# Kernel tuning notes

Hardware: AMD Instinct MI355X
Metric: run time of the kernel (lower is better)

Reference implementation:

```python
import jax, jax.numpy as jnp
import numpy as np

EPS = 1e-6  # EPSILON in the original (undefined there; small stabilizer)
MS = 1      # max_shift_size
FEAT = 128  # memory_feature_size


def setup_inputs() -> dict:
    key = jax.random.key(0)
    ks = jax.random.split(key, 17)
    B, V, E, H, N, F = 64, 10000, 256, 512, 8192, FEAT
    G = 4 * H
    s = 0.02  # param init scale
    return {
        'x': jax.random.randint(ks[0], (B,), 0, V),
        'h': jax.random.normal(ks[1], (B, H)) * 0.1,
        'c': jax.random.normal(ks[2], (B, H)) * 0.1,
        'w_read': jax.random.uniform(ks[3], (B, N)),
        'w_write': jax.random.uniform(ks[4], (B, N)),
        'bank': jax.random.normal(ks[5], (B, N, F)),
        'emb': jax.random.normal(ks[6], (V, E)) * s,
        'W_ih': jax.random.normal(ks[7], (G, E)) * s,
        'b_ih': jnp.zeros((G,)),
        'W_hh': jax.random.normal(ks[8], (G, H)) * s,
        'b_hh': jnp.zeros((G,)),
        'W_read': jax.random.normal(ks[9], (134, H)) * s,
        'b_read': jnp.zeros((134,)),
        'W_write': jax.random.normal(ks[10], (390, H)) * s,
        'b_write': jnp.zeros((390,)),
        'W_out': jax.random.normal(ks[11], (V, F)) * s,
        'b_out': jnp.zeros((V,)),
    }


def _lstm_cell(xe, h, c, W_ih, b_ih, W_hh, b_hh):
    g = xe @ W_ih.T + b_ih + h @ W_hh.T + b_hh  # [B, 4H]
    i, f, gg, o = jnp.split(g, 4, axis=1)
    c2 = jax.nn.sigmoid(f) * c + jax.nn.sigmoid(i) * jnp.tanh(gg)
    h2 = jax.nn.sigmoid(o) * jnp.tanh(c2)
    return h2, c2


def _head_move(bank, w_prev, k, b, g, s, r):
    # content addressing: cosine similarity of key vs each memory row
    mE = bank + EPS                       # [B, N, F]
    kE = k[:, None, :] + EPS              # [B, 1, F]
    num = jnp.sum(mE * kE, axis=-1)       # [B, N]
    den = jnp.linalg.norm(mE, axis=-1) * jnp.linalg.norm(kE, axis=-1)
    sim = num / jnp.maximum(den, 1e-8)
    w = jax.nn.softmax(b * sim, axis=1)
    # interpolation (as written in the source: w + (1-g)*w_prev)
    w = w + (1.0 - g) * w_prev
    # circular shift by location addressing (vectorized conv over modulo pad)
    N = w.shape[1]
    idx = (jnp.arange(N)[:, None] + jnp.arange(-MS, MS + 1)[None, :]) % N  # [N, K]
    w = jnp.einsum('bnk,bk->bn', w[:, idx], s)
    # sharpen
    wr = w ** r
    return wr / (jnp.sum(wr, axis=1, keepdims=True) + EPS)


def _interpret_read(h, W, b):
    o = h @ W.T + b
    F = FEAT
    k = o[:, :F]
    beta = jax.nn.softplus(o[:, F:F + 1])
    g = jax.nn.sigmoid(o[:, F + 1:F + 2])
    s = jax.nn.softmax(o[:, F + 2:F + 2 + (2 * MS + 1)], axis=1)
    r = 1.0 + jax.nn.softplus(o[:, F + 2 + (2 * MS + 1):F + 3 + (2 * MS + 1)])
    return k, beta, g, s, r


def _interpret_write(h, W, b):
    o = h @ W.T + b
    F = FEAT
    k, beta, g, s, r = _interpret_read(h, W[:F + 3 + (2 * MS + 1)], b[:F + 3 + (2 * MS + 1)])
    base = F + 3 + (2 * MS + 1)
    e = jax.nn.sigmoid(o[:, base:base + F])
    a = o[:, base + F:base + 2 * F]
    return k, beta, g, s, r, e, a


def reference(x, h, c, w_read, w_write, bank, emb, W_ih, b_ih, W_hh, b_hh,
              W_read, b_read, W_write, b_write, W_out, b_out):
    # controller
    xe = emb[x]                                  # [B, E]
    h2, c2 = _lstm_cell(xe, h, c, W_ih, b_ih, W_hh, b_hh)
    # write head + memory write
    k, beta, g, s, r, e, a = _interpret_write(h2, W_write, b_write)
    ww = _head_move(bank, w_write, k, beta, g, s, r)   # [B, N]
    bank2 = bank * (1.0 - ww[:, :, None] * e[:, None, :]) + ww[:, :, None] * a[:, None, :]
    # read head + memory read (uses updated bank)
    k, beta, g, s, r = _interpret_read(h2, W_read, b_read)
    wr = _head_move(bank2, w_read, k, beta, g, s, r)
    rvec = jnp.sum(wr[:, :, None] * bank2, axis=1)     # [B, F]
    return rvec @ W_out.T + b_out                      # [B, V]
```

## Files before the change

kernel.cpp:

```cpp
#include <hip/hip_runtime.h>
#include <math.h>

#define BB   64
#define NN   8192
#define FF   128
#define HH   512
#define GG   2048
#define EE   256
#define VV   10000
#define EPSF 1e-6f

static constexpr size_t OFF_XT    = 0;
static constexpr size_t OFF_GPART = 49152;
static constexpr size_t OFF_H2T   = 311296;
static constexpr size_t OFF_HPART = 344064;
static constexpr size_t OFF_PAR   = 411136;
static constexpr size_t OFF_ZW    = 445952;
static constexpr size_t OFF_Q4    = 970240;
static constexpr size_t OFF_Q1    = 3067392;
static constexpr size_t OFF_WR    = 3591680;
static constexpr size_t OFF_WRWW  = 4115968;
static constexpr size_t OFF_PT    = 4640256;
static constexpr size_t OFF_T3    = 5164544;
static constexpr size_t OFF_RVEC  = 5164608;

__device__ __forceinline__ float sigmoidf_(float x){ return 1.f/(1.f + __expf(-x)); }
__device__ __forceinline__ float softplusf_(float x){ return (x > 20.f) ? x : log1pf(__expf(x)); }

__global__ __launch_bounds__(256) void gather_xt_kernel(
    const int* __restrict__ x, const float* __restrict__ h,
    const float* __restrict__ emb, float* __restrict__ Xt)
{
  const int idx = blockIdx.x*256 + threadIdx.x;
  const int k = idx >> 6, b = idx & 63;
  float v = (k < EE) ? emb[(size_t)x[b]*EE + k] : h[(size_t)b*HH + (k - EE)];
  Xt[(size_t)k*64 + b] = v;
}

__global__ __launch_bounds__(256) void lstm_gates_kernel(
    const float* __restrict__ Xt, const float* __restrict__ Wih,
    const float* __restrict__ Whh, float* __restrict__ gpart)
{
  const int tid = threadIdx.x;
  const int lane = tid & 63;
  const int gw = __builtin_amdgcn_readfirstlane(blockIdx.x*4 + (tid >> 6));
  const int jg = gw >> 1, kc = gw & 1;
  const int j0 = jg << 2;
  float a0=0.f, a1=0.f, a2=0.f, a3=0.f;
  if (kc == 0){
    const float* w0 = Wih + (size_t)(j0+0)*EE;
    const float* w1 = Wih + (size_t)(j0+1)*EE;
    const float* w2 = Wih + (size_t)(j0+2)*EE;
    const float* w3 = Wih + (size_t)(j0+3)*EE;
    #pragma unroll 4
    for (int k = 0; k < EE; ++k){
      const float xv = Xt[(size_t)k*64 + lane];
      a0 = fmaf(w0[k],xv,a0); a1 = fmaf(w1[k],xv,a1);
      a2 = fmaf(w2[k],xv,a2); a3 = fmaf(w3[k],xv,a3);
    }
    const float* v0 = Whh + (size_t)(j0+0)*HH;
    const float* v1 = Whh + (size_t)(j0+1)*HH;
    const float* v2 = Whh + (size_t)(j0+2)*HH;
    const float* v3 = Whh + (size_t)(j0+3)*HH;
    #pragma unroll 4
    for (int k = 0; k < 128; ++k){
      const float xv = Xt[(size_t)(EE+k)*64 + lane];
      a0 = fmaf(v0[k],xv,a0); a1 = fmaf(v1[k],xv,a1);
      a2 = fmaf(v2[k],xv,a2); a3 = fmaf(v3[k],xv,a3);
    }
  } else {
    const float* v0 = Whh + (size_t)(j0+0)*HH;
    const float* v1 = Whh + (size_t)(j0+1)*HH;
    const float* v2 = Whh + (size_t)(j0+2)*HH;
    const float* v3 = Whh + (size_t)(j0+3)*HH;
    #pragma unroll 4
    for (int k = 128; k < 512; ++k){
      const float xv = Xt[(size_t)(EE+k)*64 + lane];
      a0 = fmaf(v0[k],xv,a0); a1 = fmaf(v1[k],xv,a1);
      a2 = fmaf(v2[k],xv,a2); a3 = fmaf(v3[k],xv,a3);
    }
  }
  float* gp = gpart + (size_t)kc*131072 + (size_t)j0*64 + lane;
  gp[0] = a0; gp[64] = a1; gp[128] = a2; gp[192] = a3;
}

__global__ __launch_bounds__(256) void lstm_act_kernel(
    const float* __restrict__ gpart, const float* __restrict__ bih,
    const float* __restrict__ bhh, const float* __restrict__ c,
    float* __restrict__ h2t)
{
  const int idx = blockIdx.x*256 + threadIdx.x;
  const int bb = idx & 63, hh = idx >> 6;
  #define GSUM(j) (gpart[(size_t)(j)*64+bb] + gpart[(size_t)131072+(size_t)(j)*64+bb] + bih[j] + bhh[j])
  const float gi = GSUM(hh);
  const float gf = GSUM(512+hh);
  const float gg = GSUM(1024+hh);
  const float go = GSUM(1536+hh);
  #undef GSUM
  const float c0 = c[(size_t)bb*HH + hh];
  const float c2 = sigmoidf_(gf)*c0 + sigmoidf_(gi)*tanhf(gg);
  h2t[(size_t)hh*64 + bb] = sigmoidf_(go)*tanhf(c2);
}

__global__ __launch_bounds__(256) void head_gemm_kernel(
    const float* __restrict__ h2t, const float* __restrict__ Ww,
    const float* __restrict__ Wr, float* __restrict__ hpart)
{
  const int tid = threadIdx.x;
  const int lane = tid & 63;
  const int gw = __builtin_amdgcn_readfirstlane(blockIdx.x*4 + (tid >> 6));
  const int jg = gw >> 1, kc = gw & 1;
  if (jg >= 131) return;
  const int j0 = jg << 2;
  const float* w0 = (j0+0 < 390) ? (Ww + (size_t)(j0+0)*HH) : (Wr + (size_t)(j0+0-390)*HH);
  const float* w1 = (j0+1 < 390) ? (Ww + (size_t)(j0+1)*HH) : (Wr + (size_t)(j0+1-390)*HH);
  const float* w2 = (j0+2 < 390) ? (Ww + (size_t)(j0+2)*HH) : (Wr + (size_t)(j0+2-390)*HH);
  const float* w3 = (j0+3 < 390) ? (Ww + (size_t)(j0+3)*HH) : (Wr + (size_t)(j0+3-390)*HH);
  const int k0 = kc << 8;
  float a0=0.f, a1=0.f, a2=0.f, a3=0.f;
  #pragma unroll 4
  for (int k = k0; k < k0+256; ++k){
    const float xv = h2t[(size_t)k*64 + lane];
    a0 = fmaf(w0[k],xv,a0); a1 = fmaf(w1[k],xv,a1);
    a2 = fmaf(w2[k],xv,a2); a3 = fmaf(w3[k],xv,a3);
  }
  float* hp = hpart + (size_t)kc*33536 + (size_t)j0*64 + lane;
  hp[0] = a0; hp[64] = a1; hp[128] = a2; hp[192] = a3;
}

__global__ void interpret_kernel(const float* __restrict__ hp,
                                 const float* __restrict__ bw,
                                 const float* __restrict__ br,
                                 float* __restrict__ params)
{
  const int b = blockIdx.x, l = threadIdx.x;
  float* P = params + (size_t)b*544;
  #define OC(j) (hp[(size_t)(j)*64+b] + hp[(size_t)33536+(size_t)(j)*64+b])
  float skw = 0.f, skr = 0.f, sakr = 0.f, sa2 = 0.f;
  #pragma unroll
  for (int f = l; f < 128; f += 64){
    float kwE = OC(f) + bw[f] + EPSF;
    float ee  = sigmoidf_(OC(134+f) + bw[134+f]);
    float aa  = OC(262+f) + bw[262+f];
    float krE = OC(390+f) + br[f] + EPSF;
    P[f] = kwE; P[128+f] = krE; P[256+f] = aa; P[384+f] = ee;
    skw = fmaf(kwE,kwE,skw); skr = fmaf(krE,krE,skr);
    sakr = fmaf(aa,krE,sakr); sa2 = fmaf(aa,aa,sa2);
  }
  #pragma unroll
  for (int m = 32; m >= 1; m >>= 1){
    skw += __shfl_xor(skw,m); skr += __shfl_xor(skr,m);
    sakr += __shfl_xor(sakr,m); sa2 += __shfl_xor(sa2,m);
  }
  if (l == 0){
    P[512+0] = softplusf_(OC(128) + bw[128]);
    P[512+1] = sigmoidf_(OC(129) + bw[129]);
    {
      float x0 = OC(130)+bw[130], x1 = OC(131)+bw[131], x2 = OC(132)+bw[132];
      float mm = fmaxf(x0, fmaxf(x1, x2));
      float e0 = __expf(x0-mm), e1 = __expf(x1-mm), e2 = __expf(x2-mm);
      float s = e0+e1+e2;
      P[512+2] = e0/s; P[512+3] = e1/s; P[512+4] = e2/s;
    }
    P[512+5] = 1.f + softplusf_(OC(133) + bw[133]);
    P[512+6] = softplusf_(OC(518) + br[128]);
    P[512+7] = sigmoidf_(OC(519) + br[129]);
    {
      float x0 = OC(520)+br[130], x1 = OC(521)+br[131], x2 = OC(522)+br[132];
      float mm = fmaxf(x0, fmaxf(x1, x2));
      float e0 = __expf(x0-mm), e1 = __expf(x1-mm), e2 = __expf(x2-mm);
      float s = e0+e1+e2;
      P[512+8] = e0/s; P[512+9] = e1/s; P[512+10] = e2/s;
    }
    P[512+11] = 1.f + softplusf_(OC(523) + br[133]);
    P[512+12] = sqrtf(skw); P[512+13] = sqrtf(skr);
    P[512+14] = sakr;       P[512+15] = sa2;
  }
  #undef OC
}

__global__ __launch_bounds__(256) void pass_a_kernel(
    const float* __restrict__ bank, const float* __restrict__ params,
    float* __restrict__ zw, float4* __restrict__ q4, float* __restrict__ q1)
{
  const int blk = blockIdx.x;
  const int b = blk >> 5, chunk = blk & 31;
  const int tid = threadIdx.x;
  const int wv = tid >> 6, lane = tid & 63;
  const int fslot = lane & 7, rsub = lane >> 3;
  const float* P = params + (size_t)b*544;
  const int fb = fslot << 4;
  float kw[16], kr[16], av[16], ev[16];
  #pragma unroll
  for (int i = 0; i < 16; ++i){
    kw[i] = P[fb+i]; kr[i] = P[128+fb+i]; av[i] = P[256+fb+i]; ev[i] = P[384+fb+i];
  }
  const float beta_w = P[512+0], nkw = P[512+12];
  const float C_akr = P[512+14], Ca2 = P[512+15];
  for (int it = 0; it < 8; ++it){
    const int n = (chunk << 8) + (it << 5) + (wv << 3) + rsub;
    const size_t row = (size_t)b*NN + n;
    const float4* m4 = reinterpret_cast<const float4*>(bank + row*FF + fb);
    float mv[16];
    *reinterpret_cast<float4*>(&mv[0])  = m4[0];
    *reinterpret_cast<float4*>(&mv[4])  = m4[1];
    *reinterpret_cast<float4*>(&mv[8])  = m4[2];
    *reinterpret_cast<float4*>(&mv[12]) = m4[3];
    float s1=0.f,s2=0.f,s3=0.f,s4=0.f,s5=0.f,s6=0.f,s7=0.f,s8=0.f;
    #pragma unroll
    for (int i = 0; i < 16; ++i){
      const float m = mv[i], u = m + EPSF, em = ev[i]*m;
      s1 = fmaf(u,kw[i],s1);  s2 = fmaf(u,u,s2);
      s3 = fmaf(u,kr[i],s3);  s4 = fmaf(em,kr[i],s4);
      s5 = fmaf(u,av[i],s5);  s6 = fmaf(u,em,s6);
      s7 = fmaf(av[i],em,s7); s8 = fmaf(em,em,s8);
    }
    #pragma unroll
    for (int mm = 1; mm < 8; mm <<= 1){
      s1 += __shfl_xor(s1,mm); s2 += __shfl_xor(s2,mm);
      s3 += __shfl_xor(s3,mm); s4 += __shfl_xor(s4,mm);
      s5 += __shfl_xor(s5,mm); s6 += __shfl_xor(s6,mm);
      s7 += __shfl_xor(s7,mm); s8 += __shfl_xor(s8,mm);
    }
    if (fslot == 0){
      float sim = s1 / fmaxf(sqrtf(s2)*nkw, 1e-8f);
      zw[row] = beta_w * sim;
      q4[row] = make_float4(s2, s3, C_akr - s4, s5 - s6);
      q1[row] = Ca2 - 2.f*s7 + s8;
    }
  }
}

__device__ __forceinline__ float blockMax1024(float v, float* red, int tid){
  #pragma unroll
  for (int m = 32; m >= 1; m >>= 1) v = fmaxf(v, __shfl_xor(v,m));
  __syncthreads();
  if ((tid & 63) == 0) red[tid >> 6] = v;
  __syncthreads();
  if (tid == 0){
    float r = red[0];
    #pragma unroll
    for (int i = 1; i < 16; ++i) r = fmaxf(r, red[i]);
    red[16] = r;
  }
  __syncthreads();
  return red[16];
}
__device__ __forceinline__ float blockSum1024(float v, float* red, int tid){
  #pragma unroll
  for (int m = 32; m >= 1; m >>= 1) v += __shfl_xor(v,m);
  __syncthreads();
  if ((tid & 63) == 0) red[tid >> 6] = v;
  __syncthreads();
  if (tid == 0){
    float r = 0.f;
    #pragma unroll
    for (int i = 0; i < 16; ++i) r += red[i];
    red[16] = r;
  }
  __syncthreads();
  return red[16];
}

__global__ __launch_bounds__(1024) void head_pipeline_kernel(
    const float* __restrict__ zw, const float4* __restrict__ q4,
    const float* __restrict__ q1,
    const float* __restrict__ w_write, const float* __restrict__ w_read,
    const float* __restrict__ params,
    float* __restrict__ wrg, float* __restrict__ wrwwg, float* __restrict__ T3g)
{
  __shared__ float wa[NN];
  __shared__ float red[32];
  const int b = blockIdx.x;
  const int tid = threadIdx.x;
  const float* P = params + (size_t)b*544 + 512;
  const float g_w = P[1], sw0 = P[2], sw1 = P[3], sw2 = P[4], r_w = P[5];
  const float beta_r = P[6], g_r = P[7], sr0 = P[8], sr1 = P[9], sr2 = P[10], r_r = P[11];
  const float nkr = P[13];
  const size_t base = (size_t)b*NN;
  float cv[8], wwreg[8];

  float lm = -1e30f;
  #pragma unroll
  for (int i = 0; i < 8; ++i){ int n = tid + (i<<10); float z = zw[base+n]; wa[n] = z; lm = fmaxf(lm,z); }
  float M = blockMax1024(lm, red, tid);
  float ls = 0.f;
  #pragma unroll
  for (int i = 0; i < 8; ++i){ int n = tid + (i<<10); float e = __expf(wa[n]-M); wa[n] = e; ls += e; }
  float S = blockSum1024(ls, red, tid);
  const float invS = 1.f/S;
  #pragma unroll
  for (int i = 0; i < 8; ++i){ int n = tid + (i<<10); wa[n] = wa[n]*invS + (1.f-g_w)*w_write[base+n]; }
  __syncthreads();
  #pragma unroll
  for (int i = 0; i < 8; ++i){ int n = tid + (i<<10);
    cv[i] = sw0*wa[(n+NN-1)&(NN-1)] + sw1*wa[n] + sw2*wa[(n+1)&(NN-1)]; }
  __syncthreads();
  float lp = 0.f;
  #pragma unroll
  for (int i = 0; i < 8; ++i){ int n = tid + (i<<10); float p = __expf(r_w*__logf(cv[i])); wa[n] = p; lp += p; }
  float Sp = blockSum1024(lp, red, tid);
  float inv = 1.f/(Sp + EPSF);
  #pragma unroll
  for (int i = 0; i < 8; ++i){ wwreg[i] = wa[tid + (i<<10)]*inv; }
  __syncthreads();

  lm = -1e30f;
  #pragma unroll
  for (int i = 0; i < 8; ++i){
    int n = tid + (i<<10);
    const size_t row = base + n;
    const float4 q = q4[row];
    const float qq = q1[row];
    float ww = wwreg[i];
    float num = q.y + ww*q.z;
    float d2  = q.x + 2.f*ww*q.w + ww*ww*qq;
    float den = sqrtf(d2)*nkr;
    float z = beta_r * (num / fmaxf(den, 1e-8f));
    wa[n] = z; lm = fmaxf(lm,z);
  }
  M = blockMax1024(lm, red, tid);
  ls = 0.f;
  #pragma unroll
  for (int i = 0; i < 8; ++i){ int n = tid + (i<<10); float e = __expf(wa[n]-M); wa[n] = e; ls += e; }
  S = blockSum1024(ls, red, tid);
  const float invS2 = 1.f/S;
  #pragma unroll
  for (int i = 0; i < 8; ++i){ int n = tid + (i<<10); wa[n] = wa[n]*invS2 + (1.f-g_r)*w_read[base+n]; }
  __syncthreads();
  #pragma unroll
  for (int i = 0; i < 8; ++i){ int n = tid + (i<<10);
    cv[i] = sr0*wa[(n+NN-1)&(NN-1)] + sr1*wa[n] + sr2*wa[(n+1)&(NN-1)]; }
  __syncthreads();
  lp = 0.f;
  #pragma unroll
  for (int i = 0; i < 8; ++i){ int n = tid + (i<<10); float p = __expf(r_r*__logf(cv[i])); wa[n] = p; lp += p; }
  Sp = blockSum1024(lp, red, tid);
  inv = 1.f/(Sp + EPSF);
  float t3 = 0.f;
  #pragma unroll
  for (int i = 0; i < 8; ++i){
    int n = tid + (i<<10);
    float wr_ = wa[n]*inv;
    wrg[base+n] = wr_;
    float xx = wr_*wwreg[i];
    wrwwg[base+n] = xx;
    t3 += xx;
  }
  float T3 = blockSum1024(t3, red, tid);
  if (tid == 0) T3g[b] = T3;
}

__global__ __launch_bounds__(256) void pass_d_kernel(
    const float* __restrict__ bank, const float* __restrict__ wrg,
    const float* __restrict__ wrwwg, float* __restrict__ pT)
{
  const int blk = 2047 - blockIdx.x;
  const int b = blk >> 5, chunk = blk & 31;
  const int tid = threadIdx.x;
  const int st = tid >> 5, li = tid & 31;
  float4 a1 = make_float4(0.f,0.f,0.f,0.f);
  float4 a2 = make_float4(0.f,0.f,0.f,0.f);
  for (int it = 31; it >= 0; --it){
    const int n = (chunk << 8) + (it << 3) + st;
    const size_t row = (size_t)b*NN + n;
    const float w1 = wrg[row], w2 = wrwwg[row];
    const float4 m = reinterpret_cast<const float4*>(bank + row*FF)[li];
    a1.x = fmaf(w1,m.x,a1.x); a1.y = fmaf(w1,m.y,a1.y);
    a1.z = fmaf(w1,m.z,a1.z); a1.w = fmaf(w1,m.w,a1.w);
    a2.x = fmaf(w2,m.x,a2.x); a2.y = fmaf(w2,m.y,a2.y);
    a2.z = fmaf(w2,m.z,a2.z); a2.w = fmaf(w2,m.w,a2.w);
  }
  __shared__ float lds[8*256];
  *reinterpret_cast<float4*>(&lds[st*256 + li*4]) = a1;
  *reinterpret_cast<float4*>(&lds[st*256 + 128 + li*4]) = a2;
  __syncthreads();
  float s = 0.f;
  #pragma unroll
  for (int k = 0; k < 8; ++k) s += lds[k*256 + tid];
  pT[(size_t)blk*256 + tid] = s;
}

__global__ __launch_bounds__(256) void rvec_kernel(
    const float* __restrict__ pT, const float* __restrict__ params,
    const float* __restrict__ T3g, float* __restrict__ rvec)
{
  const int gid = blockIdx.x*256 + threadIdx.x;
  const int b = gid >> 7, f = gid & 127;
  float t1 = 0.f, t2 = 0.f;
  for (int cc = 0; cc < 32; ++cc){
    const float* p = pT + (size_t)((b<<5) + cc)*256;
    t1 += p[f]; t2 += p[128+f];
  }
  const float* P = params + (size_t)b*544;
  rvec[gid] = t1 - P[384+f]*t2 + P[256+f]*T3g[b];
}

__global__ __launch_bounds__(256) void out_gemm_kernel(
    const float* __restrict__ rvec, const float* __restrict__ Wout,
    const float* __restrict__ bout, float* __restrict__ out)
{
  const int tid = threadIdx.x;
  const int wv = __builtin_amdgcn_readfirstlane(tid >> 6);
  const int lane = tid & 63;
  const int j0 = blockIdx.x*32 + wv*8;
  float acc[8];
  #pragma unroll
  for (int jj = 0; jj < 8; ++jj){ int j = j0 + jj; acc[jj] = (j < VV) ? bout[j] : 0.f; }
  for (int fc = 0; fc < 128; fc += 32){
    float rv[32];
    #pragma unroll
    for (int i = 0; i < 32; ++i) rv[i] = rvec[lane*128 + fc + i];
    #pragma unroll
    for (int jj = 0; jj < 8; ++jj){
      const int j = j0 + jj;
      if (j < VV){
        const float* w = Wout + (size_t)j*128 + fc;
        #pragma unroll
        for (int i = 0; i < 32; ++i) acc[jj] = fmaf(w[i], rv[i], acc[jj]);
      }
    }
  }
  #pragma unroll
  for (int jj = 0; jj < 8; ++jj){
    int j = j0 + jj;
    if (j < VV) out[(size_t)lane*VV + j] = acc[jj];
  }
}

extern "C" void kernel_launch(void* const* d_in, const int* in_sizes, int n_in,
                              void* d_out, int out_size, void* d_ws, size_t ws_size,
                              hipStream_t stream)
{
  const int*   x       = (const int*)  d_in[0];
  const float* h       = (const float*)d_in[1];
  const float* c       = (const float*)d_in[2];
  const float* w_read  = (const float*)d_in[3];
  const float* w_write = (const float*)d_in[4];
  const float* bank    = (const float*)d_in[5];
  const float* emb     = (const float*)d_in[6];
  const float* Wih     = (const float*)d_in[7];
  const float* bih     = (const float*)d_in[8];
  const float* Whh     = (const float*)d_in[9];
  const float* bhh     = (const float*)d_in[10];
  const float* Wr      = (const float*)d_in[11];
  const float* br      = (const float*)d_in[12];
  const float* Ww      = (const float*)d_in[13];
  const float* bw      = (const float*)d_in[14];
  const float* Wout    = (const float*)d_in[15];
  const float* bout    = (const float*)d_in[16];
  float* out = (float*)d_out;
  float* ws  = (float*)d_ws;

  float* Xt    = ws + OFF_XT;
  float* gpart = ws + OFF_GPART;
  float* h2t   = ws + OFF_H2T;
  float* hpart = ws + OFF_HPART;
  float* par   = ws + OFF_PAR;
  float* zwp   = ws + OFF_ZW;
  float4* q4p  = reinterpret_cast<float4*>(ws + OFF_Q4);
  float* q1p   = ws + OFF_Q1;
  float* wrp   = ws + OFF_WR;
  float* wrwwp = ws + OFF_WRWW;
  float* pTp   = ws + OFF_PT;
  float* T3p   = ws + OFF_T3;
  float* rvp   = ws + OFF_RVEC;

  hipLaunchKernelGGL(gather_xt_kernel,     dim3(192),  dim3(256), 0, stream, x, h, emb, Xt);
  hipLaunchKernelGGL(lstm_gates_kernel,    dim3(256),  dim3(256), 0, stream, Xt, Wih, Whh, gpart);
  hipLaunchKernelGGL(lstm_act_kernel,      dim3(128),  dim3(256), 0, stream, gpart, bih, bhh, c, h2t);
  hipLaunchKernelGGL(head_gemm_kernel,     dim3(66),   dim3(256), 0, stream, h2t, Ww, Wr, hpart);
  hipLaunchKernelGGL(interpret_kernel,     dim3(64),   dim3(64),  0, stream, hpart, bw, br, par);
  hipLaunchKernelGGL(pass_a_kernel,        dim3(2048), dim3(256), 0, stream, bank, par, zwp, q4p, q1p);
  hipLaunchKernelGGL(head_pipeline_kernel, dim3(64),   dim3(1024),0, stream, zwp, q4p, q1p, w_write, w_read, par, wrp, wrwwp, T3p);
  hipLaunchKernelGGL(pass_d_kernel,        dim3(2048), dim3(256), 0, stream, bank, wrp, wrwwp, pTp);
  hipLaunchKernelGGL(rvec_kernel,          dim3(32),   dim3(256), 0, stream, pTp, par, T3p, rvp);
  hipLaunchKernelGGL(out_gemm_kernel,      dim3(313),  dim3(256), 0, stream, rvp, Wout, bout, out);
}
```

Baseline: 209.1 us.

## Fuse LSTM stages and interpret kernel into neighbors, pack read weights, use nontemporal IO

```diff
diff --git a/kernel.cpp b/kernel.cpp
--- a/kernel.cpp
+++ b/kernel.cpp
@@ -10,96 +10,70 @@
 #define VV   10000
 #define EPSF 1e-6f
 
-static constexpr size_t OFF_XT    = 0;
-static constexpr size_t OFF_GPART = 49152;
-static constexpr size_t OFF_H2T   = 311296;
-static constexpr size_t OFF_HPART = 344064;
-static constexpr size_t OFF_PAR   = 411136;
-static constexpr size_t OFF_ZW    = 445952;
-static constexpr size_t OFF_Q4    = 970240;
-static constexpr size_t OFF_Q1    = 3067392;
-static constexpr size_t OFF_WR    = 3591680;
-static constexpr size_t OFF_WRWW  = 4115968;
-static constexpr size_t OFF_PT    = 4640256;
-static constexpr size_t OFF_T3    = 5164544;
-static constexpr size_t OFF_RVEC  = 5164608;
+typedef float f4 __attribute__((ext_vector_type(4)));
+typedef float f2 __attribute__((ext_vector_type(2)));
+
+static constexpr size_t OFF_H2T   = 0;
+static constexpr size_t OFF_HPART = 32768;
+static constexpr size_t OFF_ZW    = 99840;
+static constexpr size_t OFF_Q4    = 624128;
+static constexpr size_t OFF_Q1    = 2721280;
+static constexpr size_t OFF_WRP   = 3245568;
+static constexpr size_t OFF_PT    = 4294144;
+static constexpr size_t OFF_T3    = 4818432;
+static constexpr size_t OFF_RVEC  = 4818496;
 
 __device__ __forceinline__ float sigmoidf_(float x){ return 1.f/(1.f + __expf(-x)); }
 __device__ __forceinline__ float softplusf_(float x){ return (x > 20.f) ? x : log1pf(__expf(x)); }
 
-__global__ __launch_bounds__(256) void gather_xt_kernel(
+__global__ __launch_bounds__(256) void lstm_fused_kernel(
     const int* __restrict__ x, const float* __restrict__ h,
-    const float* __restrict__ emb, float* __restrict__ Xt)
-{
-  const int idx = blockIdx.x*256 + threadIdx.x;
-  const int k = idx >> 6, b = idx & 63;
-  float v = (k < EE) ? emb[(size_t)x[b]*EE + k] : h[(size_t)b*HH + (k - EE)];
-  Xt[(size_t)k*64 + b] = v;
-}
-
-__global__ __launch_bounds__(256) void lstm_gates_kernel(
-    const float* __restrict__ Xt, const float* __restrict__ Wih,
-    const float* __restrict__ Whh, float* __restrict__ gpart)
-{
-  const int tid = threadIdx.x;
-  const int lane = tid & 63;
-  const int gw = __builtin_amdgcn_readfirstlane(blockIdx.x*4 + (tid >> 6));
-  const int jg = gw >> 1, kc = gw & 1;
-  const int j0 = jg << 2;
+    const float* __restrict__ c, const float* __restrict__ emb,
+    const float* __restrict__ Wih, const float* __restrict__ bih,
+    const float* __restrict__ Whh, const float* __restrict__ bhh,
+    float* __restrict__ h2t)
+{
+  const int lane = threadIdx.x & 63;
+  const int hh = __builtin_amdgcn_readfirstlane(blockIdx.x*4 + (threadIdx.x >> 6));
+  const int xrow = x[lane];
+  const float* xe = emb + (size_t)xrow*EE;
+  const float* hb = h   + (size_t)lane*HH;
+  const float* wi0 = Wih + (size_t)(hh       )*EE;
+  const float* wi1 = Wih + (size_t)(hh +  512)*EE;
+  const float* wi2 = Wih + (size_t)(hh + 1024)*EE;
+  const float* wi3 = Wih + (size_t)(hh + 1536)*EE;
   float a0=0.f, a1=0.f, a2=0.f, a3=0.f;
-  if (kc == 0){
-    const float* w0 = Wih + (size_t)(j0+0)*EE;
-    const float* w1 = Wih + (size_t)(j0+1)*EE;
-    const float* w2 = Wih + (size_t)(j0+2)*EE;
-    const float* w3 = Wih + (size_t)(j0+3)*EE;
-    #pragma unroll 4
-    for (int k = 0; k < EE; ++k){
-      const float xv = Xt[(size_t)k*64 + lane];
-      a0 = fmaf(w0[k],xv,a0); a1 = fmaf(w1[k],xv,a1);
-      a2 = fmaf(w2[k],xv,a2); a3 = fmaf(w3[k],xv,a3);
-    }
-    const float* v0 = Whh + (size_t)(j0+0)*HH;
-    const float* v1 = Whh + (size_t)(j0+1)*HH;
-    const float* v2 = Whh + (size_t)(j0+2)*HH;
-    const float* v3 = Whh + (size_t)(j0+3)*HH;
-    #pragma unroll 4
-    for (int k = 0; k < 128; ++k){
-      const float xv = Xt[(size_t)(EE+k)*64 + lane];
-      a0 = fmaf(v0[k],xv,a0); a1 = fmaf(v1[k],xv,a1);
-      a2 = fmaf(v2[k],xv,a2); a3 = fmaf(v3[k],xv,a3);
-    }
-  } else {
-    const float* v0 = Whh + (size_t)(j0+0)*HH;
-    const float* v1 = Whh + (size_t)(j0+1)*HH;
-    const float* v2 = Whh + (size_t)(j0+2)*HH;
-    const float* v3 = Whh + (size_t)(j0+3)*HH;
-    #pragma unroll 4
-    for (int k = 128; k < 512; ++k){
-      const float xv = Xt[(size_t)(EE+k)*64 + lane];
-      a0 = fmaf(v0[k],xv,a0); a1 = fmaf(v1[k],xv,a1);
-      a2 = fmaf(v2[k],xv,a2); a3 = fmaf(v3[k],xv,a3);
-    }
-  }
-  float* gp = gpart + (size_t)kc*131072 + (size_t)j0*64 + lane;
-  gp[0] = a0; gp[64] = a1; gp[128] = a2; gp[192] = a3;
-}
-
-__global__ __launch_bounds__(256) void lstm_act_kernel(
-    const float* __restrict__ gpart, const float* __restrict__ bih,
-    const float* __restrict__ bhh, const float* __restrict__ c,
-    float* __restrict__ h2t)
-{
-  const int idx = blockIdx.x*256 + threadIdx.x;
-  const int bb = idx & 63, hh = idx >> 6;
-  #define GSUM(j) (gpart[(size_t)(j)*64+bb] + gpart[(size_t)131072+(size_t)(j)*64+bb] + bih[j] + bhh[j])
-  const float gi = GSUM(hh);
-  const float gf = GSUM(512+hh);
-  const float gg = GSUM(1024+hh);
-  const float go = GSUM(1536+hh);
-  #undef GSUM
-  const float c0 = c[(size_t)bb*HH + hh];
+  #pragma unroll 4
+  for (int k4 = 0; k4 < EE/4; ++k4){
+    const f4 xv = reinterpret_cast<const f4*>(xe)[k4];
+    #pragma unroll
+    for (int i = 0; i < 4; ++i){
+      const int k = k4*4 + i;
+      a0 = fmaf(wi0[k], xv[i], a0); a1 = fmaf(wi1[k], xv[i], a1);
+      a2 = fmaf(wi2[k], xv[i], a2); a3 = fmaf(wi3[k], xv[i], a3);
+    }
+  }
+  const float* wh0 = Whh + (size_t)(hh       )*HH;
+  const float* wh1 = Whh + (size_t)(hh +  512)*HH;
+  const float* wh2 = Whh + (size_t)(hh + 1024)*HH;
+  const float* wh3 = Whh + (size_t)(hh + 1536)*HH;
+  #pragma unroll 4
+  for (int k4 = 0; k4 < HH/4; ++k4){
+    const f4 hv = reinterpret_cast<const f4*>(hb)[k4];
+    #pragma unroll
+    for (int i = 0; i < 4; ++i){
+      const int k = k4*4 + i;
+      a0 = fmaf(wh0[k], hv[i], a0); a1 = fmaf(wh1[k], hv[i], a1);
+      a2 = fmaf(wh2[k], hv[i], a2); a3 = fmaf(wh3[k], hv[i], a3);
+    }
+  }
+  const float gi = a0 + bih[hh]      + bhh[hh];
+  const float gf = a1 + bih[512+hh]  + bhh[512+hh];
+  const float gg = a2 + bih[1024+hh] + bhh[1024+hh];
+  const float go = a3 + bih[1536+hh] + bhh[1536+hh];
+  const float c0 = c[(size_t)lane*HH + hh];
   const float c2 = sigmoidf_(gf)*c0 + sigmoidf_(gi)*tanhf(gg);
-  h2t[(size_t)hh*64 + bb] = sigmoidf_(go)*tanhf(c2);
+  h2t[(size_t)hh*64 + lane] = sigmoidf_(go)*tanhf(c2);
 }
 
 __global__ __launch_bounds__(256) void head_gemm_kernel(
@@ -128,84 +102,60 @@
   hp[0] = a0; hp[64] = a1; hp[128] = a2; hp[192] = a3;
 }
 
-__global__ void interpret_kernel(const float* __restrict__ hp,
-                                 const float* __restrict__ bw,
-                                 const float* __restrict__ br,
-                                 float* __restrict__ params)
-{
-  const int b = blockIdx.x, l = threadIdx.x;
-  float* P = params + (size_t)b*544;
-  #define OC(j) (hp[(size_t)(j)*64+b] + hp[(size_t)33536+(size_t)(j)*64+b])
-  float skw = 0.f, skr = 0.f, sakr = 0.f, sa2 = 0.f;
-  #pragma unroll
-  for (int f = l; f < 128; f += 64){
-    float kwE = OC(f) + bw[f] + EPSF;
-    float ee  = sigmoidf_(OC(134+f) + bw[134+f]);
-    float aa  = OC(262+f) + bw[262+f];
-    float krE = OC(390+f) + br[f] + EPSF;
-    P[f] = kwE; P[128+f] = krE; P[256+f] = aa; P[384+f] = ee;
-    skw = fmaf(kwE,kwE,skw); skr = fmaf(krE,krE,skr);
-    sakr = fmaf(aa,krE,sakr); sa2 = fmaf(aa,aa,sa2);
-  }
-  #pragma unroll
-  for (int m = 32; m >= 1; m >>= 1){
-    skw += __shfl_xor(skw,m); skr += __shfl_xor(skr,m);
-    sakr += __shfl_xor(sakr,m); sa2 += __shfl_xor(sa2,m);
-  }
-  if (l == 0){
-    P[512+0] = softplusf_(OC(128) + bw[128]);
-    P[512+1] = sigmoidf_(OC(129) + bw[129]);
-    {
-      float x0 = OC(130)+bw[130], x1 = OC(131)+bw[131], x2 = OC(132)+bw[132];
-      float mm = fmaxf(x0, fmaxf(x1, x2));
-      float e0 = __expf(x0-mm), e1 = __expf(x1-mm), e2 = __expf(x2-mm);
-      float s = e0+e1+e2;
-      P[512+2] = e0/s; P[512+3] = e1/s; P[512+4] = e2/s;
-    }
-    P[512+5] = 1.f + softplusf_(OC(133) + bw[133]);
-    P[512+6] = softplusf_(OC(518) + br[128]);
-    P[512+7] = sigmoidf_(OC(519) + br[129]);
-    {
-      float x0 = OC(520)+br[130], x1 = OC(521)+br[131], x2 = OC(522)+br[132];
-      float mm = fmaxf(x0, fmaxf(x1, x2));
-      float e0 = __expf(x0-mm), e1 = __expf(x1-mm), e2 = __expf(x2-mm);
-      float s = e0+e1+e2;
-      P[512+8] = e0/s; P[512+9] = e1/s; P[512+10] = e2/s;
-    }
-    P[512+11] = 1.f + softplusf_(OC(523) + br[133]);
-    P[512+12] = sqrtf(skw); P[512+13] = sqrtf(skr);
-    P[512+14] = sakr;       P[512+15] = sa2;
-  }
-  #undef OC
-}
+#define OCJ(j) (hp[(size_t)(j)*64 + b] + hp[(size_t)33536 + (size_t)(j)*64 + b])
 
 __global__ __launch_bounds__(256) void pass_a_kernel(
-    const float* __restrict__ bank, const float* __restrict__ params,
-    float* __restrict__ zw, float4* __restrict__ q4, float* __restrict__ q1)
-{
+    const float* __restrict__ bank, const float* __restrict__ hp,
+    const float* __restrict__ bw, const float* __restrict__ br,
+    float* __restrict__ zw, f4* __restrict__ q4, float* __restrict__ q1)
+{
+  __shared__ float sKw[128], sKr[128], sA[128], sE[128];
+  __shared__ float sred[8];
   const int blk = blockIdx.x;
   const int b = blk >> 5, chunk = blk & 31;
   const int tid = threadIdx.x;
+
+  float pkw = 0.f, pakr = 0.f, pa2 = 0.f;
+  if (tid < 128){
+    const int f = tid;
+    const float kwE = OCJ(f)     + bw[f]     + EPSF;
+    const float ee  = sigmoidf_(OCJ(134+f) + bw[134+f]);
+    const float aa  = OCJ(262+f) + bw[262+f];
+    const float krE = OCJ(390+f) + br[f]     + EPSF;
+    sKw[f] = kwE; sKr[f] = krE; sA[f] = aa; sE[f] = ee;
+    pkw = kwE*kwE; pakr = aa*krE; pa2 = aa*aa;
+  }
+  #pragma unroll
+  for (int m = 32; m >= 1; m >>= 1){
+    pkw += __shfl_xor(pkw,m); pakr += __shfl_xor(pakr,m); pa2 += __shfl_xor(pa2,m);
+  }
+  if (tid == 0)  { sred[0] = pkw; sred[2] = pakr; sred[4] = pa2; }
+  if (tid == 64) { sred[1] = pkw; sred[3] = pakr; sred[5] = pa2; }
+  if (tid == 128) sred[6] = softplusf_(OCJ(128) + bw[128]);
+  __syncthreads();
+  const float nkw    = sqrtf(sred[0] + sred[1]);
+  const float C_akr  = sred[2] + sred[3];
+  const float Ca2    = sred[4] + sred[5];
+  const float beta_w = sred[6];
+
   const int wv = tid >> 6, lane = tid & 63;
   const int fslot = lane & 7, rsub = lane >> 3;
-  const float* P = params + (size_t)b*544;
   const int fb = fslot << 4;
   float kw[16], kr[16], av[16], ev[16];
   #pragma unroll
   for (int i = 0; i < 16; ++i){
-    kw[i] = P[fb+i]; kr[i] = P[128+fb+i]; av[i] = P[256+fb+i]; ev[i] = P[384+fb+i];
-  }
-  const float beta_w = P[512+0], nkw = P[512+12];
-  const float C_akr = P[512+14], Ca2 = P[512+15];
+    kw[i] = sKw[fb+i]; kr[i] = sKr[fb+i]; av[i] = sA[fb+i]; ev[i] = sE[fb+i];
+  }
+
   for (int it = 0; it < 8; ++it){
     const int n = (chunk << 8) + (it << 5) + (wv << 3) + rsub;
     const size_t row = (size_t)b*NN + n;
-    const float4* m4 = reinterpret_cast<const float4*>(bank + row*FF + fb);
+    const f4* m4 = reinterpret_cast<const f4*>(bank + row*FF + fb);
     float mv[16];
-    *reinterpret_cast<float4*>(&mv[0])  = m4[0];
-    *reinterpret_cast<float4*>(&mv[4])  = m4[1];
-    *reinterpret_cast<float4*>(&mv[8])  = m4[2];
-    *reinterpret_cast<float4*>(&mv[12]) = m4[3];
+    *reinterpret_cast<f4*>(&mv[0])  = m4[0];
+    *reinterpret_cast<f4*>(&mv[4])  = m4[1];
+    *reinterpret_cast<f4*>(&mv[8])  = m4[2];
+    *reinterpret_cast<f4*>(&mv[12]) = m4[3];
     float s1=0.f,s2=0.f,s3=0.f,s4=0.f,s5=0.f,s6=0.f,s7=0.f,s8=0.f;
     #pragma unroll
     for (int i = 0; i < 16; ++i){
@@ -223,10 +173,11 @@
       s7 += __shfl_xor(s7,mm); s8 += __shfl_xor(s8,mm);
     }
     if (fslot == 0){
-      float sim = s1 / fmaxf(sqrtf(s2)*nkw, 1e-8f);
-      zw[row] = beta_w * sim;
-      q4[row] = make_float4(s2, s3, C_akr - s4, s5 - s6);
-      q1[row] = Ca2 - 2.f*s7 + s8;
+      const float sim = s1 / fmaxf(sqrtf(s2)*nkw, 1e-8f);
+      __builtin_nontemporal_store(beta_w * sim, &zw[row]);
+      f4 qv; qv[0] = s2; qv[1] = s3; qv[2] = C_akr - s4; qv[3] = s5 - s6;
+      __builtin_nontemporal_store(qv, &q4[row]);
+      __builtin_nontemporal_store(Ca2 - 2.f*s7 + s8, &q1[row]);
     }
   }
 }
@@ -263,26 +214,58 @@
 }
 
 __global__ __launch_bounds__(1024) void head_pipeline_kernel(
-    const float* __restrict__ zw, const float4* __restrict__ q4,
+    const float* __restrict__ zw, const f4* __restrict__ q4,
     const float* __restrict__ q1,
     const float* __restrict__ w_write, const float* __restrict__ w_read,
-    const float* __restrict__ params,
-    float* __restrict__ wrg, float* __restrict__ wrwwg, float* __restrict__ T3g)
+    const float* __restrict__ hp, const float* __restrict__ bw,
+    const float* __restrict__ br,
+    f2* __restrict__ wrpair, float* __restrict__ T3g)
 {
   __shared__ float wa[NN];
   __shared__ float red[32];
+  __shared__ float sS[14];
   const int b = blockIdx.x;
   const int tid = threadIdx.x;
-  const float* P = params + (size_t)b*544 + 512;
-  const float g_w = P[1], sw0 = P[2], sw1 = P[3], sw2 = P[4], r_w = P[5];
-  const float beta_r = P[6], g_r = P[7], sr0 = P[8], sr1 = P[9], sr2 = P[10], r_r = P[11];
-  const float nkr = P[13];
+
+  float pnkr = 0.f;
+  if (tid < 128){
+    const float krE = OCJ(390+tid) + br[tid] + EPSF;
+    pnkr = krE*krE;
+  }
+  #pragma unroll
+  for (int m = 32; m >= 1; m >>= 1) pnkr += __shfl_xor(pnkr,m);
+  if (tid == 0)  red[20] = pnkr;
+  if (tid == 64) red[21] = pnkr;
+  if (tid == 128){
+    sS[1] = sigmoidf_(OCJ(129) + bw[129]);
+    float x0 = OCJ(130)+bw[130], x1 = OCJ(131)+bw[131], x2 = OCJ(132)+bw[132];
+    float mm = fmaxf(x0, fmaxf(x1, x2));
+    float e0 = __expf(x0-mm), e1 = __expf(x1-mm), e2 = __expf(x2-mm);
+    float s = e0+e1+e2;
+    sS[2] = e0/s; sS[3] = e1/s; sS[4] = e2/s;
+    sS[5] = 1.f + softplusf_(OCJ(133) + bw[133]);
+  }
+  if (tid == 129){
+    sS[6] = softplusf_(OCJ(518) + br[128]);
+    sS[7] = sigmoidf_(OCJ(519) + br[129]);
+    float x0 = OCJ(520)+br[130], x1 = OCJ(521)+br[131], x2 = OCJ(522)+br[132];
+    float mm = fmaxf(x0, fmaxf(x1, x2));
+    float e0 = __expf(x0-mm), e1 = __expf(x1-mm), e2 = __expf(x2-mm);
+    float s = e0+e1+e2;
+    sS[8] = e0/s; sS[9] = e1/s; sS[10] = e2/s;
+    sS[11] = 1.f + softplusf_(OCJ(523) + br[133]);
+  }
+  __syncthreads();
+  const float g_w = sS[1], sw0 = sS[2], sw1 = sS[3], sw2 = sS[4], r_w = sS[5];
+  const float beta_r = sS[6], g_r = sS[7], sr0 = sS[8], sr1 = sS[9], sr2 = sS[10], r_r = sS[11];
+  const float nkr = sqrtf(red[20] + red[21]);
   const size_t base = (size_t)b*NN;
   float cv[8], wwreg[8];
 
   float lm = -1e30f;
   #pragma unroll
-  for (int i = 0; i < 8; ++i){ int n = tid + (i<<10); float z = zw[base+n]; wa[n] = z; lm = fmaxf(lm,z); }
+  for (int i = 0; i < 8; ++i){ int n = tid + (i<<10);
+    float z = __builtin_nontemporal_load(&zw[base+n]); wa[n] = z; lm = fmaxf(lm,z); }
   float M = blockMax1024(lm, red, tid);
   float ls = 0.f;
   #pragma unroll
@@ -290,7 +273,8 @@
   float S = blockSum1024(ls, red, tid);
   const float invS = 1.f/S;
   #pragma unroll
-  for (int i = 0; i < 8; ++i){ int n = tid + (i<<10); wa[n] = wa[n]*invS + (1.f-g_w)*w_write[base+n]; }
+  for (int i = 0; i < 8; ++i){ int n = tid + (i<<10);
+    wa[n] = wa[n]*invS + (1.f-g_w)*__builtin_nontemporal_load(&w_write[base+n]); }
   __syncthreads();
   #pragma unroll
   for (int i = 0; i < 8; ++i){ int n = tid + (i<<10);
@@ -310,11 +294,11 @@
   for (int i = 0; i < 8; ++i){
     int n = tid + (i<<10);
     const size_t row = base + n;
-    const float4 q = q4[row];
-    const float qq = q1[row];
+    const f4 q = __builtin_nontemporal_load(&q4[row]);
+    const float qq = __builtin_nontemporal_load(&q1[row]);
     float ww = wwreg[i];
-    float num = q.y + ww*q.z;
-    float d2  = q.x + 2.f*ww*q.w + ww*ww*qq;
+    float num = q[1] + ww*q[2];
+    float d2  = q[0] + 2.f*ww*q[3] + ww*ww*qq;
     float den = sqrtf(d2)*nkr;
     float z = beta_r * (num / fmaxf(den, 1e-8f));
     wa[n] = z; lm = fmaxf(lm,z);
@@ -326,7 +310,8 @@
   S = blockSum1024(ls, red, tid);
   const float invS2 = 1.f/S;
   #pragma unroll
-  for (int i = 0; i < 8; ++i){ int n = tid + (i<<10); wa[n] = wa[n]*invS2 + (1.f-g_r)*w_read[base+n]; }
+  for (int i = 0; i < 8; ++i){ int n = tid + (i<<10);
+    wa[n] = wa[n]*invS2 + (1.f-g_r)*__builtin_nontemporal_load(&w_read[base+n]); }
   __syncthreads();
   #pragma unroll
   for (int i = 0; i < 8; ++i){ int n = tid + (i<<10);
@@ -342,9 +327,9 @@
   for (int i = 0; i < 8; ++i){
     int n = tid + (i<<10);
     float wr_ = wa[n]*inv;
-    wrg[base+n] = wr_;
     float xx = wr_*wwreg[i];
-    wrwwg[base+n] = xx;
+    f2 pr; pr[0] = wr_; pr[1] = xx;
+    __builtin_nontemporal_store(pr, &wrpair[base+n]);
     t3 += xx;
   }
   float T3 = blockSum1024(t3, red, tid);
@@ -352,38 +337,40 @@
 }
 
 __global__ __launch_bounds__(256) void pass_d_kernel(
-    const float* __restrict__ bank, const float* __restrict__ wrg,
-    const float* __restrict__ wrwwg, float* __restrict__ pT)
+    const float* __restrict__ bank, const f2* __restrict__ wrpair,
+    float* __restrict__ pT)
 {
   const int blk = 2047 - blockIdx.x;
   const int b = blk >> 5, chunk = blk & 31;
   const int tid = threadIdx.x;
   const int st = tid >> 5, li = tid & 31;
-  float4 a1 = make_float4(0.f,0.f,0.f,0.f);
-  float4 a2 = make_float4(0.f,0.f,0.f,0.f);
+  f4 a1 = {0.f,0.f,0.f,0.f};
+  f4 a2 = {0.f,0.f,0.f,0.f};
   for (int it = 31; it >= 0; --it){
     const int n = (chunk << 8) + (it << 3) + st;
     const size_t row = (size_t)b*NN + n;
-    const float w1 = wrg[row], w2 = wrwwg[row];
-    const float4 m = reinterpret_cast<const float4*>(bank + row*FF)[li];
-    a1.x = fmaf(w1,m.x,a1.x); a1.y = fmaf(w1,m.y,a1.y);
-    a1.z = fmaf(w1,m.z,a1.z); a1.w = fmaf(w1,m.w,a1.w);
-    a2.x = fmaf(w2,m.x,a2.x); a2.y = fmaf(w2,m.y,a2.y);
-    a2.z = fmaf(w2,m.z,a2.z); a2.w = fmaf(w2,m.w,a2.w);
+    const f2 w = __builtin_nontemporal_load(&wrpair[row]);
+    const f4 m = reinterpret_cast<const f4*>(bank + row*FF)[li];
+    #pragma unroll
+    for (int cc = 0; cc < 4; ++cc){
+      a1[cc] = fmaf(w[0], m[cc], a1[cc]);
+      a2[cc] = fmaf(w[1], m[cc], a2[cc]);
+    }
   }
   __shared__ float lds[8*256];
-  *reinterpret_cast<float4*>(&lds[st*256 + li*4]) = a1;
-  *reinterpret_cast<float4*>(&lds[st*256 + 128 + li*4]) = a2;
+  *reinterpret_cast<f4*>(&lds[st*256 + li*4]) = a1;
+  *reinterpret_cast<f4*>(&lds[st*256 + 128 + li*4]) = a2;
   __syncthreads();
   float s = 0.f;
   #pragma unroll
   for (int k = 0; k < 8; ++k) s += lds[k*256 + tid];
-  pT[(size_t)blk*256 + tid] = s;
+  __builtin_nontemporal_store(s, &pT[(size_t)blk*256 + tid]);
 }
 
 __global__ __launch_bounds__(256) void rvec_kernel(
-    const float* __restrict__ pT, const float* __restrict__ params,
-    const float* __restrict__ T3g, float* __restrict__ rvec)
+    const float* __restrict__ pT, const float* __restrict__ hp,
+    const float* __restrict__ bw, const float* __restrict__ T3g,
+    float* __restrict__ rvec)
 {
   const int gid = blockIdx.x*256 + threadIdx.x;
   const int b = gid >> 7, f = gid & 127;
@@ -392,8 +379,9 @@
     const float* p = pT + (size_t)((b<<5) + cc)*256;
     t1 += p[f]; t2 += p[128+f];
   }
-  const float* P = params + (size_t)b*544;
-  rvec[gid] = t1 - P[384+f]*t2 + P[256+f]*T3g[b];
+  const float ee = sigmoidf_(OCJ(134+f) + bw[134+f]);
+  const float aa = OCJ(262+f) + bw[262+f];
+  rvec[gid] = t1 - ee*t2 + aa*T3g[b];
 }
 
 __global__ __launch_bounds__(256) void out_gemm_kernel(
@@ -452,28 +440,28 @@
   float* out = (float*)d_out;
   float* ws  = (float*)d_ws;
 
-  float* Xt    = ws + OFF_XT;
-  float* gpart = ws + OFF_GPART;
   float* h2t   = ws + OFF_H2T;
   float* hpart = ws + OFF_HPART;
-  float* par   = ws + OFF_PAR;
   float* zwp   = ws + OFF_ZW;
-  float4* q4p  = reinterpret_cast<float4*>(ws + OFF_Q4);
+  f4*    q4p   = reinterpret_cast<f4*>(ws + OFF_Q4);
   float* q1p   = ws + OFF_Q1;
-  float* wrp   = ws + OFF_WR;
-  float* wrwwp = ws + OFF_WRWW;
+  f2*    wrp   = reinterpret_cast<f2*>(ws + OFF_WRP);
   float* pTp   = ws + OFF_PT;
   float* T3p   = ws + OFF_T3;
   float* rvp   = ws + OFF_RVEC;
 
-  hipLaunchKernelGGL(gather_xt_kernel,     dim3(192),  dim3(256), 0, stream, x, h, emb, Xt);
-  hipLaunchKernelGGL(lstm_gates_kernel,    dim3(256),  dim3(256), 0, stream, Xt, Wih, Whh, gpart);
-  hipLaunchKernelGGL(lstm_act_kernel,      dim3(128),  dim3(256), 0, stream, gpart, bih, bhh, c, h2t);
-  hipLaunchKernelGGL(head_gemm_kernel,     dim3(66),   dim3(256), 0, stream, h2t, Ww, Wr, hpart);
-  hipLaunchKernelGGL(interpret_kernel,     dim3(64),   dim3(64),  0, stream, hpart, bw, br, par);
-  hipLaunchKernelGGL(pass_a_kernel,        dim3(2048), dim3(256), 0, stream, bank, par, zwp, q4p, q1p);
-  hipLaunchKernelGGL(head_pipeline_kernel, dim3(64),   dim3(1024),0, stream, zwp, q4p, q1p, w_write, w_read, par, wrp, wrwwp, T3p);
-  hipLaunchKernelGGL(pass_d_kernel,        dim3(2048), dim3(256), 0, stream, bank, wrp, wrwwp, pTp);
-  hipLaunchKernelGGL(rvec_kernel,          dim3(32),   dim3(256), 0, stream, pTp, par, T3p, rvp);
-  hipLaunchKernelGGL(out_gemm_kernel,      dim3(313),  dim3(256), 0, stream, rvp, Wout, bout, out);
-}
+  hipLaunchKernelGGL(lstm_fused_kernel,    dim3(128),  dim3(256), 0, stream,
+                     x, h, c, emb, Wih, bih, Whh, bhh, h2t);
+  hipLaunchKernelGGL(head_gemm_kernel,     dim3(66),   dim3(256), 0, stream,
+                     h2t, Ww, Wr, hpart);
+  hipLaunchKernelGGL(pass_a_kernel,        dim3(2048), dim3(256), 0, stream,
+                     bank, hpart, bw, br, zwp, q4p, q1p);
+  hipLaunchKernelGGL(head_pipeline_kernel, dim3(64),   dim3(1024),0, stream,
+                     zwp, q4p, q1p, w_write, w_read, hpart, bw, br, wrp, T3p);
+  hipLaunchKernelGGL(pass_d_kernel,        dim3(2048), dim3(256), 0, stream,
+                     bank, wrp, pTp);
+  hipLaunchKernelGGL(rvec_kernel,          dim3(32),   dim3(256), 0, stream,
+                     pTp, hpart, bw, T3p, rvp);
+  hipLaunchKernelGGL(out_gemm_kernel,      dim3(313),  dim3(256), 0, stream,
+                     rvp, Wout, bout, out);
+}
```

Measured after the change: 227.3 us. 1.09x slower.
